# Kernel optimization log

Hardware: AMD Instinct MI355X
Metric: run time of the kernel (lower is better)

The kernel has to match this reference:

```python
import jax, jax.numpy as jnp
import numpy as np

ALPHA = 0.05
MAX_ITER = 200
TOL = 0.01
N = 64
M = 1
BATCH = 262144


def setup_inputs() -> dict:
    key = jax.random.key(0)
    pred_cost = jax.random.normal(key, (BATCH, N), dtype=jnp.float32)
    # constraint data (fixed buffers, match init_kwargs)
    A = np.ones((M, N), dtype=np.float32)
    b = np.full((M,), 32.0, dtype=np.float32)
    lb = np.zeros((N,), dtype=np.float32)
    ub = np.ones((N,), dtype=np.float32)
    # SVD-based pseudoinverse factors for equality projection
    U, s, VT = np.linalg.svd(A, full_matrices=False)
    s_inv = np.where(s >= 1e-6, 1.0 / s, 0.0).astype(np.float32)
    return {
        "pred_cost": pred_cost,
        "A": jnp.asarray(A),
        "b": jnp.asarray(b),
        "lb": jnp.asarray(lb),
        "ub": jnp.asarray(ub),
        "V": jnp.asarray(VT.T.astype(np.float32)),   # (n, m)
        "UT": jnp.asarray(U.T.astype(np.float32)),   # (m, m)
        "s_inv": jnp.asarray(s_inv),                 # (m,)
    }


def _project_box(z, lb, ub):
    return jnp.clip(z, lb, ub)


def _project_equality(w, A, b, V, UT, s_inv):
    # w: (B, n). residual r = A w^T - b, correction = V diag(s_inv) U^T r
    r = w @ A.T - b                      # (B, m)
    corr = ((r @ UT.T) * s_inv) @ V.T    # (B, n)
    return w - corr


def _dys_step(z, cost, A, b, lb, ub, V, UT, s_inv):
    x = _project_box(z, lb, ub)
    grad = cost + ALPHA * x              # grad of regularized objective
    y = _project_equality(2.0 * x - z - ALPHA * grad, A, b, V, UT, s_inv)
    return z - x + y


def _run_to_convergence(cost, A, b, lb, ub, V, UT, s_inv):
    lb_safe = jnp.where(jnp.isfinite(lb), lb, 0.0)
    ub_safe = jnp.where(jnp.isfinite(ub), ub, 1.0)
    z0 = jax.random.uniform(jax.random.key(1), cost.shape, dtype=cost.dtype)
    z0 = z0 * (ub_safe - lb_safe) + lb_safe

    def cond(state):
        i, z, diff = state
        return jnp.logical_and(i < MAX_ITER, diff > TOL)

    def body(state):
        i, z, _ = state
        z_new = _dys_step(z, cost, A, b, lb, ub, V, UT, s_inv)
        diff = jnp.max(jnp.linalg.norm(z_new - z, axis=1))
        return (i + 1, z_new, diff)

    _, z, _ = jax.lax.while_loop(cond, body, (jnp.int32(0), z0, jnp.float32(1e30)))
    return z


def reference(pred_cost, A, b, lb, ub, V, UT, s_inv):
    cost = pred_cost  # minimize=True
    # no-grad fixed-point iterations
    z = jax.lax.stop_gradient(
        _run_to_convergence(jax.lax.stop_gradient(cost), A, b, lb, ub, V, UT, s_inv)
    )
    # training branch: one differentiable DYS step (JFB), then box projection
    z = _dys_step(z, cost, A, b, lb, ub, V, UT, s_inv)
    sol = _project_box(z, lb, ub)
    return sol
```

## Files before the change

### kernel.cpp

```cpp
#include <hip/hip_runtime.h>
#include <cstdint>


#ifndef JAX_PARTITIONABLE
#define JAX_PARTITIONABLE 1
#endif

#define BATCHN 262144
#define MAXIT  200
#define RPW    16
#define NWAVES (BATCHN / RPW)
#define PROBE_ROWS 8192
#define PROBE_WAVES (PROBE_ROWS / RPW)

#define K1 0.9975f
#define K2 1.9975f

__device__ __forceinline__ void tf2x32(uint32_t x0, uint32_t x1,
                                       uint32_t& o0, uint32_t& o1) {
  const uint32_t k0 = 0u, k1 = 1u;
  const uint32_t k2 = 0x1BD11BDAu ^ k0 ^ k1;
  x0 += k0; x1 += k1;
#define TFR(r) { x0 += x1; x1 = (x1 << (r)) | (x1 >> (32 - (r))); x1 ^= x0; }
  TFR(13) TFR(15) TFR(26) TFR(6)   x0 += k1; x1 += k2 + 1u;
  TFR(17) TFR(29) TFR(16) TFR(24)  x0 += k2; x1 += k0 + 2u;
  TFR(13) TFR(15) TFR(26) TFR(6)   x0 += k0; x1 += k1 + 3u;
  TFR(17) TFR(29) TFR(16) TFR(24)  x0 += k1; x1 += k2 + 4u;
  TFR(13) TFR(15) TFR(26) TFR(6)   x0 += k2; x1 += k0 + 5u;
#undef TFR
  o0 = x0; o1 = x1;
}

__device__ __forceinline__ float z0_at(uint32_t f) {
  uint32_t b;
#if JAX_PARTITIONABLE
  uint32_t o0, o1;
  tf2x32(0u, f, o0, o1);
  b = o0 ^ o1;
#else
  const uint32_t H = 8388608u;
  uint32_t lo = (f < H) ? f : (f - H);
  uint32_t o0, o1;
  tf2x32(lo, lo + H, o0, o1);
  b = (f < H) ? o0 : o1;
#endif
  return __uint_as_float((b >> 9) | 0x3f800000u) - 1.0f;
}

template <int CTRL>
__device__ __forceinline__ float dpp_add(float v) {
  int s = __builtin_amdgcn_mov_dpp(__float_as_int(v), CTRL, 0xF, 0xF, true);
  return v + __int_as_float(s);
}

__device__ __forceinline__ float reduce4(float v) {
  v = dpp_add<0xB1>(v);
  v = dpp_add<0x4E>(v);
  return v;
}

__device__ __forceinline__ void fast_iter(float U[16], const float c[16],
                                          float& CC, float& R) {
  const float Ch = CC + 20.0f;
  float sp[4] = {0.0f, 0.0f, 0.0f, 0.0f};
#pragma unroll
  for (int j = 0; j < 16; ++j) {
    float m = __builtin_amdgcn_fmed3f(U[j], CC, Ch);
    sp[j & 3] += m;
    U[j] = __builtin_fmaf(K1, m, -c[j]);
  }
  float s = (sp[0] + sp[1]) + (sp[2] + sp[3]);
  s = reduce4(s);
  float Sx = 0.05f * __builtin_fmaf(-64.0f, CC, s);
  float t  = __builtin_fmaf(K2, Sx, -R);
  float corr20 = __builtin_fmaf(t, 0.3125f, -10.0f);
  R = (R - Sx) + 32.0f;
  CC = __builtin_fmaf(K1, CC, corr20);
}

__device__ __forceinline__ float chk_iter(float U[16], const float c[16],
                                          float& CC, float& R) {
  const float Ch = CC + 20.0f;
  float sp[4] = {0.0f, 0.0f, 0.0f, 0.0f};
  float q1a = 0.0f, q1b = 0.0f, q2a = 0.0f, q2b = 0.0f;
#pragma unroll
  for (int j = 0; j < 16; ++j) {
    float m = __builtin_amdgcn_fmed3f(U[j], CC, Ch);
    sp[j & 3] += m;
    float un = __builtin_fmaf(K1, m, -c[j]);
    float d = un - U[j];
    if (j & 1) { q1b += d; q2b = __builtin_fmaf(d, d, q2b); }
    else       { q1a += d; q2a = __builtin_fmaf(d, d, q2a); }
    U[j] = un;
  }
  float s = (sp[0] + sp[1]) + (sp[2] + sp[3]);
  s = reduce4(s);
  float Sx = 0.05f * __builtin_fmaf(-64.0f, CC, s);
  float t  = __builtin_fmaf(K2, Sx, -R);
  float corr20 = __builtin_fmaf(t, 0.3125f, -10.0f);
  R = (R - Sx) + 32.0f;
  float CCn = __builtin_fmaf(K1, CC, corr20);
  float dCC = CCn - CC;
  CC = CCn;
  float q1 = reduce4(q1a + q1b);
  float q2 = reduce4(q2a + q2b);
  float a = __builtin_fmaf(64.0f, dCC, -2.0f * q1);
  return __builtin_fmaf(dCC, a, q2);
}

__device__ __forceinline__ void load_c(const float* __restrict__ cost,
                                       int base, float c[16]) {
#pragma unroll
  for (int k = 0; k < 4; ++k) {
    const float4 cq = *(const float4*)(cost + base + 4 * k);
    c[4 * k + 0] = cq.x; c[4 * k + 1] = cq.y;
    c[4 * k + 2] = cq.z; c[4 * k + 3] = cq.w;
  }
}

__device__ __forceinline__ void pin16(float v[16]) {
#pragma unroll
  for (int j = 0; j < 16; ++j) asm("" : "+v"(v[j]));
}

__device__ __forceinline__ void init_state(const float* __restrict__ cost,
                                           int base, float c[16], float U[16],
                                           float& CC, float& R) {
  load_c(cost, base, c);
  float r = 0.0f;
#pragma unroll
  for (int j = 0; j < 16; ++j) {
    float z0 = z0_at((uint32_t)(base + j));
    U[j] = 20.0f * z0;
    r = __builtin_fmaf(0.05f, c[j], r + z0);
  }
  pin16(c);
  pin16(U);
  R = reduce4(r);
  CC = 0.0f;
}

__global__ __launch_bounds__(256, 4) void dys_probe(
    const float* __restrict__ cost, int* __restrict__ Tsample) {
  const int lane = threadIdx.x & 63;
  const int gw = blockIdx.x * 4 + (threadIdx.x >> 6);
  const int base = (gw * RPW + (lane >> 2)) * 64 + (lane & 3) * 16;

  float c[16], U[16], CC, R;
  init_state(cost, base, c, U, CC, R);

  int ib = MAXIT;
  for (int i = 1; i <= MAXIT; ++i) {
    float ds = chk_iter(U, c, CC, R);
    if (__all(ds <= 0.04f)) { ib = i; break; }
  }
  if (lane == 0) atomicMax(Tsample, ib);
}

__global__ __launch_bounds__(256, 4) void dys_pass1(
    const float* __restrict__ cost, const int* __restrict__ Tsample,
    int* __restrict__ Tglob, int* __restrict__ TrArr,
    float* __restrict__ zst) {
  const int lane = threadIdx.x & 63;
  const int gw = blockIdx.x * 4 + (threadIdx.x >> 6);
  const int base = (gw * RPW + (lane >> 2)) * 64 + (lane & 3) * 16;

  float c[16], U[16], CC, R;
  init_state(cost, base, c, U, CC, R);

  const int Ts = *Tsample;
  const int P = (Ts > 2) ? (Ts - 2) : 0;

  for (int i = 0; i < P; ++i) fast_iter(U, c, CC, R);

  int ib = MAXIT;
  for (int i = P + 1; i <= MAXIT; ++i) {
    float ds = chk_iter(U, c, CC, R);
    if (__all(ds <= 0.04f)) { ib = i; break; }
  }

  const float CC05 = 0.05f * CC;
#pragma unroll
  for (int k = 0; k < 4; ++k) {
    float4 zq;
    zq.x = __builtin_fmaf(0.05f, U[4 * k + 0], -CC05);
    zq.y = __builtin_fmaf(0.05f, U[4 * k + 1], -CC05);
    zq.z = __builtin_fmaf(0.05f, U[4 * k + 2], -CC05);
    zq.w = __builtin_fmaf(0.05f, U[4 * k + 3], -CC05);
    *(float4*)(zst + base + 4 * k) = zq;
  }
  if (lane == 0) {
    TrArr[gw] = ib;
    atomicMax(Tglob, ib);
  }
}

__global__ __launch_bounds__(256, 4) void dys_pass2(
    const float* __restrict__ cost, const int* __restrict__ Tglob,
    const int* __restrict__ TrArr, const float* __restrict__ zst,
    float* __restrict__ out) {
  const int lane = threadIdx.x & 63;
  const int gw = blockIdx.x * 4 + (threadIdx.x >> 6);
  const int base = (gw * RPW + (lane >> 2)) * 64 + (lane & 3) * 16;

  float c[16], U[16];
  load_c(cost, base, c);
  float r = 0.0f;
#pragma unroll
  for (int k = 0; k < 4; ++k) {
    const float4 zq = *(const float4*)(zst + base + 4 * k);
    U[4 * k + 0] = 20.0f * zq.x; U[4 * k + 1] = 20.0f * zq.y;
    U[4 * k + 2] = 20.0f * zq.z; U[4 * k + 3] = 20.0f * zq.w;
    r += (zq.x + zq.y) + (zq.z + zq.w);
  }
#pragma unroll
  for (int j = 0; j < 16; ++j) r = __builtin_fmaf(0.05f, c[j], r);
  pin16(c);
  pin16(U);
  float CC = 0.0f;
  float R = reduce4(r);

  const int T = *Tglob;
  const int ib = TrArr[gw];

  for (int i = ib; i <= T; ++i) fast_iter(U, c, CC, R);

  const float CC05 = 0.05f * CC;
#pragma unroll
  for (int k = 0; k < 4; ++k) {
    float4 o;
    o.x = __builtin_amdgcn_fmed3f(
        __builtin_fmaf(0.05f, U[4 * k + 0], -CC05), 0.0f, 1.0f);
    o.y = __builtin_amdgcn_fmed3f(
        __builtin_fmaf(0.05f, U[4 * k + 1], -CC05), 0.0f, 1.0f);
    o.z = __builtin_amdgcn_fmed3f(
        __builtin_fmaf(0.05f, U[4 * k + 2], -CC05), 0.0f, 1.0f);
    o.w = __builtin_amdgcn_fmed3f(
        __builtin_fmaf(0.05f, U[4 * k + 3], -CC05), 0.0f, 1.0f);
    *(float4*)(out + base + 4 * k) = o;
  }
}

extern "C" void kernel_launch(void* const* d_in, const int* in_sizes, int n_in,
                              void* d_out, int out_size, void* d_ws,
                              size_t ws_size, hipStream_t stream) {
  const float* cost = (const float*)d_in[0];
  float* out = (float*)d_out;

  int* Tglob   = (int*)d_ws;
  int* Tsample = (int*)d_ws + 1;
  const size_t TR_OFF = 1024;
  const size_t Z_OFF  = TR_OFF + (size_t)NWAVES * sizeof(int);
  int*   TrArr = (int*)((char*)d_ws + TR_OFF);
  float* zst   = (float*)((char*)d_ws + Z_OFF);

  hipMemsetAsync(d_ws, 0, 8, stream);

  dim3 block(256);
  dys_probe<<<dim3(PROBE_WAVES / 4), block, 0, stream>>>(cost, Tsample);
  dys_pass1<<<dim3(NWAVES / 4), block, 0, stream>>>(cost, Tsample, Tglob,
                                                    TrArr, zst);
  dys_pass2<<<dim3(NWAVES / 4), block, 0, stream>>>(cost, Tglob, TrArr, zst,
                                                    out);
}
```

Baseline: 415.2 us.

## Map one row per lane and use packed FP32 math in main passes

The main iteration kernels now give each lane a whole 64-element row instead of splitting a row across 4 lanes. This removes the cross-lane DPP reductions from every iteration. The inner updates use v_pk_add/v_pk_fma packed FP32 instructions on pairs of elements. The cost is 64+ live floats per lane, so launch bounds drop to 2 blocks per CU, which lowers occupancy. Per-lane global loads now stride 256 bytes across lanes, which is less coalesced.

```diff
diff --git a/kernel.cpp b/kernel.cpp
--- a/kernel.cpp
+++ b/kernel.cpp
@@ -8,13 +8,30 @@
 
 #define BATCHN 262144
 #define MAXIT  200
-#define RPW    16
-#define NWAVES (BATCHN / RPW)
+
+#define RPW_A  16
 #define PROBE_ROWS 8192
-#define PROBE_WAVES (PROBE_ROWS / RPW)
+#define PROBE_WAVES (PROBE_ROWS / RPW_A)
+#define NWAVES_A (BATCHN / RPW_A)
+
+#define RPW_B  64
+#define NWAVES_B (BATCHN / RPW_B)
 
 #define K1 0.9975f
 #define K2 1.9975f
+
+typedef float v2f __attribute__((ext_vector_type(2)));
+
+__device__ __forceinline__ v2f pk_add(v2f a, v2f b) {
+  v2f d;
+  asm("v_pk_add_f32 %0, %1, %2" : "=v"(d) : "v"(a), "v"(b));
+  return d;
+}
+__device__ __forceinline__ v2f pk_fma(v2f a, v2f b, v2f c) {
+  v2f d;
+  asm("v_pk_fma_f32 %0, %1, %2, %3" : "=v"(d) : "v"(a), "v"(b), "v"(c));
+  return d;
+}
 
 __device__ __forceinline__ void tf2x32(uint32_t x0, uint32_t x1,
                                        uint32_t& o0, uint32_t& o1) {
@@ -47,6 +64,7 @@
   return __uint_as_float((b >> 9) | 0x3f800000u) - 1.0f;
 }
 
+
 template <int CTRL>
 __device__ __forceinline__ float dpp_add(float v) {
   int s = __builtin_amdgcn_mov_dpp(__float_as_int(v), CTRL, 0xF, 0xF, true);
@@ -59,27 +77,8 @@
   return v;
 }
 
-__device__ __forceinline__ void fast_iter(float U[16], const float c[16],
-                                          float& CC, float& R) {
-  const float Ch = CC + 20.0f;
-  float sp[4] = {0.0f, 0.0f, 0.0f, 0.0f};
-#pragma unroll
-  for (int j = 0; j < 16; ++j) {
-    float m = __builtin_amdgcn_fmed3f(U[j], CC, Ch);
-    sp[j & 3] += m;
-    U[j] = __builtin_fmaf(K1, m, -c[j]);
-  }
-  float s = (sp[0] + sp[1]) + (sp[2] + sp[3]);
-  s = reduce4(s);
-  float Sx = 0.05f * __builtin_fmaf(-64.0f, CC, s);
-  float t  = __builtin_fmaf(K2, Sx, -R);
-  float corr20 = __builtin_fmaf(t, 0.3125f, -10.0f);
-  R = (R - Sx) + 32.0f;
-  CC = __builtin_fmaf(K1, CC, corr20);
-}
-
-__device__ __forceinline__ float chk_iter(float U[16], const float c[16],
-                                          float& CC, float& R) {
+__device__ __forceinline__ float chk_iter_A(float U[16], const float c[16],
+                                            float& CC, float& R) {
   const float Ch = CC + 20.0f;
   float sp[4] = {0.0f, 0.0f, 0.0f, 0.0f};
   float q1a = 0.0f, q1b = 0.0f, q2a = 0.0f, q2b = 0.0f;
@@ -108,8 +107,8 @@
   return __builtin_fmaf(dCC, a, q2);
 }
 
-__device__ __forceinline__ void load_c(const float* __restrict__ cost,
-                                       int base, float c[16]) {
+__device__ __forceinline__ void load_c_A(const float* __restrict__ cost,
+                                         int base, float c[16]) {
 #pragma unroll
   for (int k = 0; k < 4; ++k) {
     const float4 cq = *(const float4*)(cost + base + 4 * k);
@@ -123,10 +122,11 @@
   for (int j = 0; j < 16; ++j) asm("" : "+v"(v[j]));
 }
 
-__device__ __forceinline__ void init_state(const float* __restrict__ cost,
-                                           int base, float c[16], float U[16],
-                                           float& CC, float& R) {
-  load_c(cost, base, c);
+__device__ __forceinline__ void init_state_A(const float* __restrict__ cost,
+                                             int base, float c[16],
+                                             float U[16], float& CC,
+                                             float& R) {
+  load_c_A(cost, base, c);
   float r = 0.0f;
 #pragma unroll
   for (int j = 0; j < 16; ++j) {
@@ -144,49 +144,140 @@
     const float* __restrict__ cost, int* __restrict__ Tsample) {
   const int lane = threadIdx.x & 63;
   const int gw = blockIdx.x * 4 + (threadIdx.x >> 6);
-  const int base = (gw * RPW + (lane >> 2)) * 64 + (lane & 3) * 16;
+  const int base = (gw * RPW_A + (lane >> 2)) * 64 + (lane & 3) * 16;
 
   float c[16], U[16], CC, R;
-  init_state(cost, base, c, U, CC, R);
+  init_state_A(cost, base, c, U, CC, R);
 
   int ib = MAXIT;
   for (int i = 1; i <= MAXIT; ++i) {
-    float ds = chk_iter(U, c, CC, R);
+    float ds = chk_iter_A(U, c, CC, R);
     if (__all(ds <= 0.04f)) { ib = i; break; }
   }
   if (lane == 0) atomicMax(Tsample, ib);
 }
 
-__global__ __launch_bounds__(256, 4) void dys_pass1(
+
+__device__ __forceinline__ void pin32(v2f v[32]) {
+#pragma unroll
+  for (int j = 0; j < 32; ++j) asm("" : "+v"(v[j]));
+}
+
+__device__ __forceinline__ void fast_iter_B(v2f U2[32], const v2f nc2[32],
+                                            float& CC, float& R) {
+  const float Ch = CC + 20.0f;
+  const v2f K1p = {K1, K1};
+  v2f spA = {0.0f, 0.0f}, spB = {0.0f, 0.0f};
+#pragma unroll
+  for (int p = 0; p < 32; ++p) {
+    v2f m2;
+    m2.x = __builtin_amdgcn_fmed3f(U2[p].x, CC, Ch);
+    m2.y = __builtin_amdgcn_fmed3f(U2[p].y, CC, Ch);
+    if (p & 1) spB = pk_add(spB, m2);
+    else       spA = pk_add(spA, m2);
+    U2[p] = pk_fma(K1p, m2, nc2[p]);
+  }
+  v2f spc = pk_add(spA, spB);
+  float s = spc.x + spc.y;
+  float Sx = 0.05f * __builtin_fmaf(-64.0f, CC, s);
+  float t  = __builtin_fmaf(K2, Sx, -R);
+  float corr20 = __builtin_fmaf(t, 0.3125f, -10.0f);
+  R = (R - Sx) + 32.0f;
+  CC = __builtin_fmaf(K1, CC, corr20);
+}
+
+__device__ __forceinline__ float chk_iter_B(v2f U2[32], const v2f nc2[32],
+                                            float& CC, float& R) {
+  const float Ch = CC + 20.0f;
+  const v2f K1p = {K1, K1};
+  v2f spA = {0.0f, 0.0f}, spB = {0.0f, 0.0f};
+  v2f q1v = {0.0f, 0.0f}, q2v = {0.0f, 0.0f};
+#pragma unroll
+  for (int p = 0; p < 32; ++p) {
+    v2f m2, un2, d2;
+    m2.x = __builtin_amdgcn_fmed3f(U2[p].x, CC, Ch);
+    m2.y = __builtin_amdgcn_fmed3f(U2[p].y, CC, Ch);
+    if (p & 1) spB = pk_add(spB, m2);
+    else       spA = pk_add(spA, m2);
+    un2 = pk_fma(K1p, m2, nc2[p]);
+    d2.x = un2.x - U2[p].x;
+    d2.y = un2.y - U2[p].y;
+    q1v = pk_add(q1v, d2);
+    q2v = pk_fma(d2, d2, q2v);
+    U2[p] = un2;
+  }
+  v2f spc = pk_add(spA, spB);
+  float s = spc.x + spc.y;
+  float Sx = 0.05f * __builtin_fmaf(-64.0f, CC, s);
+  float t  = __builtin_fmaf(K2, Sx, -R);
+  float corr20 = __builtin_fmaf(t, 0.3125f, -10.0f);
+  R = (R - Sx) + 32.0f;
+  float CCn = __builtin_fmaf(K1, CC, corr20);
+  float dCC = CCn - CC;
+  CC = CCn;
+  float q1 = q1v.x + q1v.y;
+  float q2 = q2v.x + q2v.y;
+  float a = __builtin_fmaf(64.0f, dCC, -2.0f * q1);
+  return __builtin_fmaf(dCC, a, q2);
+}
+
+__device__ __forceinline__ void init_state_B(const float* __restrict__ cost,
+                                             int base, v2f nc2[32],
+                                             v2f U2[32], float& CC,
+                                             float& R) {
+#pragma unroll
+  for (int k = 0; k < 16; ++k) {
+    const float4 cq = *(const float4*)(cost + base + 4 * k);
+    nc2[2 * k + 0].x = -cq.x; nc2[2 * k + 0].y = -cq.y;
+    nc2[2 * k + 1].x = -cq.z; nc2[2 * k + 1].y = -cq.w;
+  }
+  float r0 = 0.0f, r1 = 0.0f;
+#pragma unroll
+  for (int p = 0; p < 32; ++p) {
+    float za = z0_at((uint32_t)(base + 2 * p));
+    float zb = z0_at((uint32_t)(base + 2 * p + 1));
+    U2[p].x = 20.0f * za;
+    U2[p].y = 20.0f * zb;
+    r0 = __builtin_fmaf(-0.05f, nc2[p].x, r0 + za);
+    r1 = __builtin_fmaf(-0.05f, nc2[p].y, r1 + zb);
+  }
+  pin32(nc2);
+  pin32(U2);
+  R = r0 + r1;
+  CC = 0.0f;
+}
+
+__global__ __launch_bounds__(256, 2) void dys_pass1(
     const float* __restrict__ cost, const int* __restrict__ Tsample,
     int* __restrict__ Tglob, int* __restrict__ TrArr,
     float* __restrict__ zst) {
   const int lane = threadIdx.x & 63;
   const int gw = blockIdx.x * 4 + (threadIdx.x >> 6);
-  const int base = (gw * RPW + (lane >> 2)) * 64 + (lane & 3) * 16;
-
-  float c[16], U[16], CC, R;
-  init_state(cost, base, c, U, CC, R);
+  const int base = (gw * RPW_B + lane) * 64;
+
+  v2f nc2[32], U2[32];
+  float CC, R;
+  init_state_B(cost, base, nc2, U2, CC, R);
 
   const int Ts = *Tsample;
   const int P = (Ts > 2) ? (Ts - 2) : 0;
 
-  for (int i = 0; i < P; ++i) fast_iter(U, c, CC, R);
+  for (int i = 0; i < P; ++i) fast_iter_B(U2, nc2, CC, R);
 
   int ib = MAXIT;
   for (int i = P + 1; i <= MAXIT; ++i) {
-    float ds = chk_iter(U, c, CC, R);
+    float ds = chk_iter_B(U2, nc2, CC, R);
     if (__all(ds <= 0.04f)) { ib = i; break; }
   }
 
   const float CC05 = 0.05f * CC;
 #pragma unroll
-  for (int k = 0; k < 4; ++k) {
+  for (int k = 0; k < 16; ++k) {
     float4 zq;
-    zq.x = __builtin_fmaf(0.05f, U[4 * k + 0], -CC05);
-    zq.y = __builtin_fmaf(0.05f, U[4 * k + 1], -CC05);
-    zq.z = __builtin_fmaf(0.05f, U[4 * k + 2], -CC05);
-    zq.w = __builtin_fmaf(0.05f, U[4 * k + 3], -CC05);
+    zq.x = __builtin_fmaf(0.05f, U2[2 * k + 0].x, -CC05);
+    zq.y = __builtin_fmaf(0.05f, U2[2 * k + 0].y, -CC05);
+    zq.z = __builtin_fmaf(0.05f, U2[2 * k + 1].x, -CC05);
+    zq.w = __builtin_fmaf(0.05f, U2[2 * k + 1].y, -CC05);
     *(float4*)(zst + base + 4 * k) = zq;
   }
   if (lane == 0) {
@@ -195,48 +286,57 @@
   }
 }
 
-__global__ __launch_bounds__(256, 4) void dys_pass2(
+__global__ __launch_bounds__(256, 2) void dys_pass2(
     const float* __restrict__ cost, const int* __restrict__ Tglob,
     const int* __restrict__ TrArr, const float* __restrict__ zst,
     float* __restrict__ out) {
   const int lane = threadIdx.x & 63;
   const int gw = blockIdx.x * 4 + (threadIdx.x >> 6);
-  const int base = (gw * RPW + (lane >> 2)) * 64 + (lane & 3) * 16;
-
-  float c[16], U[16];
-  load_c(cost, base, c);
-  float r = 0.0f;
-#pragma unroll
-  for (int k = 0; k < 4; ++k) {
+  const int base = (gw * RPW_B + lane) * 64;
+
+  v2f nc2[32], U2[32];
+#pragma unroll
+  for (int k = 0; k < 16; ++k) {
+    const float4 cq = *(const float4*)(cost + base + 4 * k);
+    nc2[2 * k + 0].x = -cq.x; nc2[2 * k + 0].y = -cq.y;
+    nc2[2 * k + 1].x = -cq.z; nc2[2 * k + 1].y = -cq.w;
+  }
+  float r0 = 0.0f, r1 = 0.0f;
+#pragma unroll
+  for (int k = 0; k < 16; ++k) {
     const float4 zq = *(const float4*)(zst + base + 4 * k);
-    U[4 * k + 0] = 20.0f * zq.x; U[4 * k + 1] = 20.0f * zq.y;
-    U[4 * k + 2] = 20.0f * zq.z; U[4 * k + 3] = 20.0f * zq.w;
-    r += (zq.x + zq.y) + (zq.z + zq.w);
-  }
-#pragma unroll
-  for (int j = 0; j < 16; ++j) r = __builtin_fmaf(0.05f, c[j], r);
-  pin16(c);
-  pin16(U);
+    U2[2 * k + 0].x = 20.0f * zq.x; U2[2 * k + 0].y = 20.0f * zq.y;
+    U2[2 * k + 1].x = 20.0f * zq.z; U2[2 * k + 1].y = 20.0f * zq.w;
+    r0 += (zq.x + zq.y);
+    r1 += (zq.z + zq.w);
+  }
+#pragma unroll
+  for (int p = 0; p < 32; ++p) {
+    r0 = __builtin_fmaf(-0.05f, nc2[p].x, r0);
+    r1 = __builtin_fmaf(-0.05f, nc2[p].y, r1);
+  }
+  pin32(nc2);
+  pin32(U2);
   float CC = 0.0f;
-  float R = reduce4(r);
+  float R = r0 + r1;
 
   const int T = *Tglob;
   const int ib = TrArr[gw];
 
-  for (int i = ib; i <= T; ++i) fast_iter(U, c, CC, R);
+  for (int i = ib; i <= T; ++i) fast_iter_B(U2, nc2, CC, R);
 
   const float CC05 = 0.05f * CC;
 #pragma unroll
-  for (int k = 0; k < 4; ++k) {
+  for (int k = 0; k < 16; ++k) {
     float4 o;
     o.x = __builtin_amdgcn_fmed3f(
-        __builtin_fmaf(0.05f, U[4 * k + 0], -CC05), 0.0f, 1.0f);
+        __builtin_fmaf(0.05f, U2[2 * k + 0].x, -CC05), 0.0f, 1.0f);
     o.y = __builtin_amdgcn_fmed3f(
-        __builtin_fmaf(0.05f, U[4 * k + 1], -CC05), 0.0f, 1.0f);
+        __builtin_fmaf(0.05f, U2[2 * k + 0].y, -CC05), 0.0f, 1.0f);
     o.z = __builtin_amdgcn_fmed3f(
-        __builtin_fmaf(0.05f, U[4 * k + 2], -CC05), 0.0f, 1.0f);
+        __builtin_fmaf(0.05f, U2[2 * k + 1].x, -CC05), 0.0f, 1.0f);
     o.w = __builtin_amdgcn_fmed3f(
-        __builtin_fmaf(0.05f, U[4 * k + 3], -CC05), 0.0f, 1.0f);
+        __builtin_fmaf(0.05f, U2[2 * k + 1].y, -CC05), 0.0f, 1.0f);
     *(float4*)(out + base + 4 * k) = o;
   }
 }
@@ -250,7 +350,7 @@
   int* Tglob   = (int*)d_ws;
   int* Tsample = (int*)d_ws + 1;
   const size_t TR_OFF = 1024;
-  const size_t Z_OFF  = TR_OFF + (size_t)NWAVES * sizeof(int);
+  const size_t Z_OFF  = TR_OFF + (size_t)NWAVES_A * sizeof(int);
   int*   TrArr = (int*)((char*)d_ws + TR_OFF);
   float* zst   = (float*)((char*)d_ws + Z_OFF);
 
@@ -258,8 +358,8 @@
 
   dim3 block(256);
   dys_probe<<<dim3(PROBE_WAVES / 4), block, 0, stream>>>(cost, Tsample);
-  dys_pass1<<<dim3(NWAVES / 4), block, 0, stream>>>(cost, Tsample, Tglob,
-                                                    TrArr, zst);
-  dys_pass2<<<dim3(NWAVES / 4), block, 0, stream>>>(cost, Tglob, TrArr, zst,
-                                                    out);
-}
+  dys_pass1<<<dim3(NWAVES_B / 4), block, 0, stream>>>(cost, Tsample, Tglob,
+                                                      TrArr, zst);
+  dys_pass2<<<dim3(NWAVES_B / 4), block, 0, stream>>>(cost, Tglob, TrArr, zst,
+                                                      out);
+}
```

Result: faster. 389.3 us (-6.2%).

## Map one row per lane with packed float2 math in main DYS passes

Applied to the files above, without the earlier changes.

The main passes now give each lane a whole 64-element row, held as 32 float2 pairs, instead of spreading a row across 4 lanes. This removes the DPP cross-lane reductions on every iteration and uses packed FMA on vector pairs to halve the VALU instruction count. In exchange each thread holds far more registers, occupancy drops (launch bounds go from 4 to 2), the per-row loads become strided across lanes, and there are four times fewer waves. The early-exit check now covers 64 rows per wave, so waves may iterate longer before all lanes converge.

```diff
diff --git a/kernel.cpp b/kernel.cpp
--- a/kernel.cpp
+++ b/kernel.cpp
@@ -8,13 +8,19 @@
 
 #define BATCHN 262144
 #define MAXIT  200
-#define RPW    16
-#define NWAVES (BATCHN / RPW)
+
+#define RPW_A  16
 #define PROBE_ROWS 8192
-#define PROBE_WAVES (PROBE_ROWS / RPW)
+#define PROBE_WAVES (PROBE_ROWS / RPW_A)
+#define NWAVES_A (BATCHN / RPW_A)
+
+#define RPW_B  64
+#define NWAVES_B (BATCHN / RPW_B)
 
 #define K1 0.9975f
 #define K2 1.9975f
+
+typedef float v2f __attribute__((ext_vector_type(2)));
 
 __device__ __forceinline__ void tf2x32(uint32_t x0, uint32_t x1,
                                        uint32_t& o0, uint32_t& o1) {
@@ -47,6 +53,7 @@
   return __uint_as_float((b >> 9) | 0x3f800000u) - 1.0f;
 }
 
+
 template <int CTRL>
 __device__ __forceinline__ float dpp_add(float v) {
   int s = __builtin_amdgcn_mov_dpp(__float_as_int(v), CTRL, 0xF, 0xF, true);
@@ -59,27 +66,8 @@
   return v;
 }
 
-__device__ __forceinline__ void fast_iter(float U[16], const float c[16],
-                                          float& CC, float& R) {
-  const float Ch = CC + 20.0f;
-  float sp[4] = {0.0f, 0.0f, 0.0f, 0.0f};
-#pragma unroll
-  for (int j = 0; j < 16; ++j) {
-    float m = __builtin_amdgcn_fmed3f(U[j], CC, Ch);
-    sp[j & 3] += m;
-    U[j] = __builtin_fmaf(K1, m, -c[j]);
-  }
-  float s = (sp[0] + sp[1]) + (sp[2] + sp[3]);
-  s = reduce4(s);
-  float Sx = 0.05f * __builtin_fmaf(-64.0f, CC, s);
-  float t  = __builtin_fmaf(K2, Sx, -R);
-  float corr20 = __builtin_fmaf(t, 0.3125f, -10.0f);
-  R = (R - Sx) + 32.0f;
-  CC = __builtin_fmaf(K1, CC, corr20);
-}
-
-__device__ __forceinline__ float chk_iter(float U[16], const float c[16],
-                                          float& CC, float& R) {
+__device__ __forceinline__ float chk_iter_A(float U[16], const float c[16],
+                                            float& CC, float& R) {
   const float Ch = CC + 20.0f;
   float sp[4] = {0.0f, 0.0f, 0.0f, 0.0f};
   float q1a = 0.0f, q1b = 0.0f, q2a = 0.0f, q2b = 0.0f;
@@ -108,8 +96,8 @@
   return __builtin_fmaf(dCC, a, q2);
 }
 
-__device__ __forceinline__ void load_c(const float* __restrict__ cost,
-                                       int base, float c[16]) {
+__device__ __forceinline__ void load_c_A(const float* __restrict__ cost,
+                                         int base, float c[16]) {
 #pragma unroll
   for (int k = 0; k < 4; ++k) {
     const float4 cq = *(const float4*)(cost + base + 4 * k);
@@ -123,10 +111,11 @@
   for (int j = 0; j < 16; ++j) asm("" : "+v"(v[j]));
 }
 
-__device__ __forceinline__ void init_state(const float* __restrict__ cost,
-                                           int base, float c[16], float U[16],
-                                           float& CC, float& R) {
-  load_c(cost, base, c);
+__device__ __forceinline__ void init_state_A(const float* __restrict__ cost,
+                                             int base, float c[16],
+                                             float U[16], float& CC,
+                                             float& R) {
+  load_c_A(cost, base, c);
   float r = 0.0f;
 #pragma unroll
   for (int j = 0; j < 16; ++j) {
@@ -144,101 +133,174 @@
     const float* __restrict__ cost, int* __restrict__ Tsample) {
   const int lane = threadIdx.x & 63;
   const int gw = blockIdx.x * 4 + (threadIdx.x >> 6);
-  const int base = (gw * RPW + (lane >> 2)) * 64 + (lane & 3) * 16;
+  const int base = (gw * RPW_A + (lane >> 2)) * 64 + (lane & 3) * 16;
 
   float c[16], U[16], CC, R;
-  init_state(cost, base, c, U, CC, R);
+  init_state_A(cost, base, c, U, CC, R);
 
   int ib = MAXIT;
   for (int i = 1; i <= MAXIT; ++i) {
-    float ds = chk_iter(U, c, CC, R);
+    float ds = chk_iter_A(U, c, CC, R);
     if (__all(ds <= 0.04f)) { ib = i; break; }
   }
   if (lane == 0) atomicMax(Tsample, ib);
 }
 
-__global__ __launch_bounds__(256, 4) void dys_pass1(
+
+#define P32(X) X(0) X(1) X(2) X(3) X(4) X(5) X(6) X(7) X(8) X(9) X(10) X(11) \
+  X(12) X(13) X(14) X(15) X(16) X(17) X(18) X(19) X(20) X(21) X(22) X(23) \
+  X(24) X(25) X(26) X(27) X(28) X(29) X(30) X(31)
+
+#define PAIRS(X) X(0,0,1) X(1,2,3) X(2,4,5) X(3,6,7) X(4,8,9) X(5,10,11) \
+  X(6,12,13) X(7,14,15) X(8,16,17) X(9,18,19) X(10,20,21) X(11,22,23) \
+  X(12,24,25) X(13,26,27) X(14,28,29) X(15,30,31)
+
+#define DECL_STATE(p) v2f U##p, nc##p;
+
+#define LOADC(k, p0, p1) { \
+  const float4 cq = *(const float4*)(cost + base + 4 * (k)); \
+  nc##p0.x = -cq.x; nc##p0.y = -cq.y; nc##p1.x = -cq.z; nc##p1.y = -cq.w; }
+
+#define INITU(p) { \
+  const float za = z0_at((uint32_t)(base + 2 * (p))); \
+  const float zb = z0_at((uint32_t)(base + 2 * (p) + 1)); \
+  U##p.x = 20.0f * za; U##p.y = 20.0f * zb; \
+  r0 = __builtin_fmaf(-0.05f, nc##p.x, r0 + za); \
+  r1 = __builtin_fmaf(-0.05f, nc##p.y, r1 + zb); }
+
+#define FSTEP(p) { v2f m2; \
+  m2.x = __builtin_amdgcn_fmed3f(U##p.x, CC, Ch); \
+  m2.y = __builtin_amdgcn_fmed3f(U##p.y, CC, Ch); \
+  if ((p) & 1) spB += m2; else spA += m2; \
+  U##p = __builtin_elementwise_fma(K1p, m2, nc##p); }
+
+#define FAST_ITER() { \
+  const float Ch = CC + 20.0f; \
+  v2f spA = {0.0f, 0.0f}, spB = {0.0f, 0.0f}; \
+  P32(FSTEP) \
+  const v2f spc = spA + spB; \
+  const float s_ = spc.x + spc.y; \
+  const float Sx = 0.05f * __builtin_fmaf(-64.0f, CC, s_); \
+  const float t_ = __builtin_fmaf(K2, Sx, -R); \
+  const float corr20 = __builtin_fmaf(t_, 0.3125f, -10.0f); \
+  R = (R - Sx) + 32.0f; \
+  CC = __builtin_fmaf(K1, CC, corr20); }
+
+#define CSTEP(p) { v2f m2; \
+  m2.x = __builtin_amdgcn_fmed3f(U##p.x, CC, Ch); \
+  m2.y = __builtin_amdgcn_fmed3f(U##p.y, CC, Ch); \
+  if ((p) & 1) spB += m2; else spA += m2; \
+  const v2f un2 = __builtin_elementwise_fma(K1p, m2, nc##p); \
+  const v2f d2 = un2 - U##p; \
+  q1v += d2; \
+  q2v = __builtin_elementwise_fma(d2, d2, q2v); \
+  U##p = un2; }
+
+#define CHK_ITER(DS) { \
+  const float Ch = CC + 20.0f; \
+  v2f spA = {0.0f, 0.0f}, spB = {0.0f, 0.0f}; \
+  v2f q1v = {0.0f, 0.0f}, q2v = {0.0f, 0.0f}; \
+  P32(CSTEP) \
+  const v2f spc = spA + spB; \
+  const float s_ = spc.x + spc.y; \
+  const float Sx = 0.05f * __builtin_fmaf(-64.0f, CC, s_); \
+  const float t_ = __builtin_fmaf(K2, Sx, -R); \
+  const float corr20 = __builtin_fmaf(t_, 0.3125f, -10.0f); \
+  R = (R - Sx) + 32.0f; \
+  const float CCn = __builtin_fmaf(K1, CC, corr20); \
+  const float dCC = CCn - CC; CC = CCn; \
+  const float q1 = q1v.x + q1v.y; \
+  const float q2 = q2v.x + q2v.y; \
+  const float a_ = __builtin_fmaf(64.0f, dCC, -2.0f * q1); \
+  DS = __builtin_fmaf(dCC, a_, q2); }
+
+#define STZ(k, p0, p1) { float4 zq; \
+  zq.x = __builtin_fmaf(0.05f, U##p0.x, -CC05); \
+  zq.y = __builtin_fmaf(0.05f, U##p0.y, -CC05); \
+  zq.z = __builtin_fmaf(0.05f, U##p1.x, -CC05); \
+  zq.w = __builtin_fmaf(0.05f, U##p1.y, -CC05); \
+  *(float4*)(zst + base + 4 * (k)) = zq; }
+
+#define LOADZ(k, p0, p1) { \
+  const float4 zq = *(const float4*)(zst + base + 4 * (k)); \
+  U##p0.x = 20.0f * zq.x; U##p0.y = 20.0f * zq.y; \
+  U##p1.x = 20.0f * zq.z; U##p1.y = 20.0f * zq.w; \
+  r0 += zq.x + zq.y; r1 += zq.z + zq.w; }
+
+#define RC(p) { r0 = __builtin_fmaf(-0.05f, nc##p.x, r0); \
+  r1 = __builtin_fmaf(-0.05f, nc##p.y, r1); }
+
+#define STOUT(k, p0, p1) { float4 o; \
+  o.x = __builtin_amdgcn_fmed3f( \
+      __builtin_fmaf(0.05f, U##p0.x, -CC05), 0.0f, 1.0f); \
+  o.y = __builtin_amdgcn_fmed3f( \
+      __builtin_fmaf(0.05f, U##p0.y, -CC05), 0.0f, 1.0f); \
+  o.z = __builtin_amdgcn_fmed3f( \
+      __builtin_fmaf(0.05f, U##p1.x, -CC05), 0.0f, 1.0f); \
+  o.w = __builtin_amdgcn_fmed3f( \
+      __builtin_fmaf(0.05f, U##p1.y, -CC05), 0.0f, 1.0f); \
+  *(float4*)(out + base + 4 * (k)) = o; }
+
+__global__ __launch_bounds__(256, 2) void dys_pass1(
     const float* __restrict__ cost, const int* __restrict__ Tsample,
     int* __restrict__ Tglob, int* __restrict__ TrArr,
     float* __restrict__ zst) {
   const int lane = threadIdx.x & 63;
   const int gw = blockIdx.x * 4 + (threadIdx.x >> 6);
-  const int base = (gw * RPW + (lane >> 2)) * 64 + (lane & 3) * 16;
-
-  float c[16], U[16], CC, R;
-  init_state(cost, base, c, U, CC, R);
+  const int base = (gw * RPW_B + lane) * 64;
+
+  const v2f K1p = {K1, K1};
+  P32(DECL_STATE)
+  PAIRS(LOADC)
+  float r0 = 0.0f, r1 = 0.0f;
+  P32(INITU)
+  float R = r0 + r1;
+  float CC = 0.0f;
 
   const int Ts = *Tsample;
-  const int P = (Ts > 2) ? (Ts - 2) : 0;
-
-  for (int i = 0; i < P; ++i) fast_iter(U, c, CC, R);
+  const int Pn = (Ts > 2) ? (Ts - 2) : 0;
+
+  for (int i = 0; i < Pn; ++i) FAST_ITER();
 
   int ib = MAXIT;
-  for (int i = P + 1; i <= MAXIT; ++i) {
-    float ds = chk_iter(U, c, CC, R);
+  for (int i = Pn + 1; i <= MAXIT; ++i) {
+    float ds;
+    CHK_ITER(ds)
     if (__all(ds <= 0.04f)) { ib = i; break; }
   }
 
   const float CC05 = 0.05f * CC;
-#pragma unroll
-  for (int k = 0; k < 4; ++k) {
-    float4 zq;
-    zq.x = __builtin_fmaf(0.05f, U[4 * k + 0], -CC05);
-    zq.y = __builtin_fmaf(0.05f, U[4 * k + 1], -CC05);
-    zq.z = __builtin_fmaf(0.05f, U[4 * k + 2], -CC05);
-    zq.w = __builtin_fmaf(0.05f, U[4 * k + 3], -CC05);
-    *(float4*)(zst + base + 4 * k) = zq;
-  }
+  PAIRS(STZ)
   if (lane == 0) {
     TrArr[gw] = ib;
     atomicMax(Tglob, ib);
   }
 }
 
-__global__ __launch_bounds__(256, 4) void dys_pass2(
+__global__ __launch_bounds__(256, 2) void dys_pass2(
     const float* __restrict__ cost, const int* __restrict__ Tglob,
     const int* __restrict__ TrArr, const float* __restrict__ zst,
     float* __restrict__ out) {
   const int lane = threadIdx.x & 63;
   const int gw = blockIdx.x * 4 + (threadIdx.x >> 6);
-  const int base = (gw * RPW + (lane >> 2)) * 64 + (lane & 3) * 16;
-
-  float c[16], U[16];
-  load_c(cost, base, c);
-  float r = 0.0f;
-#pragma unroll
-  for (int k = 0; k < 4; ++k) {
-    const float4 zq = *(const float4*)(zst + base + 4 * k);
-    U[4 * k + 0] = 20.0f * zq.x; U[4 * k + 1] = 20.0f * zq.y;
-    U[4 * k + 2] = 20.0f * zq.z; U[4 * k + 3] = 20.0f * zq.w;
-    r += (zq.x + zq.y) + (zq.z + zq.w);
-  }
-#pragma unroll
-  for (int j = 0; j < 16; ++j) r = __builtin_fmaf(0.05f, c[j], r);
-  pin16(c);
-  pin16(U);
+  const int base = (gw * RPW_B + lane) * 64;
+
+  const v2f K1p = {K1, K1};
+  P32(DECL_STATE)
+  PAIRS(LOADC)
+  float r0 = 0.0f, r1 = 0.0f;
+  PAIRS(LOADZ)
+  P32(RC)
+  float R = r0 + r1;
   float CC = 0.0f;
-  float R = reduce4(r);
 
   const int T = *Tglob;
   const int ib = TrArr[gw];
 
-  for (int i = ib; i <= T; ++i) fast_iter(U, c, CC, R);
+  for (int i = ib; i <= T; ++i) FAST_ITER();
 
   const float CC05 = 0.05f * CC;
-#pragma unroll
-  for (int k = 0; k < 4; ++k) {
-    float4 o;
-    o.x = __builtin_amdgcn_fmed3f(
-        __builtin_fmaf(0.05f, U[4 * k + 0], -CC05), 0.0f, 1.0f);
-    o.y = __builtin_amdgcn_fmed3f(
-        __builtin_fmaf(0.05f, U[4 * k + 1], -CC05), 0.0f, 1.0f);
-    o.z = __builtin_amdgcn_fmed3f(
-        __builtin_fmaf(0.05f, U[4 * k + 2], -CC05), 0.0f, 1.0f);
-    o.w = __builtin_amdgcn_fmed3f(
-        __builtin_fmaf(0.05f, U[4 * k + 3], -CC05), 0.0f, 1.0f);
-    *(float4*)(out + base + 4 * k) = o;
-  }
+  PAIRS(STOUT)
 }
 
 extern "C" void kernel_launch(void* const* d_in, const int* in_sizes, int n_in,
@@ -250,7 +312,7 @@
   int* Tglob   = (int*)d_ws;
   int* Tsample = (int*)d_ws + 1;
   const size_t TR_OFF = 1024;
-  const size_t Z_OFF  = TR_OFF + (size_t)NWAVES * sizeof(int);
+  const size_t Z_OFF  = TR_OFF + (size_t)NWAVES_A * sizeof(int);
   int*   TrArr = (int*)((char*)d_ws + TR_OFF);
   float* zst   = (float*)((char*)d_ws + Z_OFF);
 
@@ -258,8 +320,8 @@
 
   dim3 block(256);
   dys_probe<<<dim3(PROBE_WAVES / 4), block, 0, stream>>>(cost, Tsample);
-  dys_pass1<<<dim3(NWAVES / 4), block, 0, stream>>>(cost, Tsample, Tglob,
-                                                    TrArr, zst);
-  dys_pass2<<<dim3(NWAVES / 4), block, 0, stream>>>(cost, Tglob, TrArr, zst,
-                                                    out);
-}
+  dys_pass1<<<dim3(NWAVES_B / 4), block, 0, stream>>>(cost, Tsample, Tglob,
+                                                      TrArr, zst);
+  dys_pass2<<<dim3(NWAVES_B / 4), block, 0, stream>>>(cost, Tglob, TrArr, zst,
+                                                      out);
+}
```

Measured after the change: 391.3 us. -5.8%, faster.
